# Optimization experiments

Measured on AMD Instinct MI355X. Metric: run time of the kernel, lower is better.

The kernel has to match this reference:

```python
import jax, jax.numpy as jnp
import numpy as np

N = 100000        # nodes
E_RAND = 1600000  # random edges (self loops appended -> E = E_RAND + N)
H = 64            # agg_hidden
IN = 7            # in_channels
L = 3             # n_layer
FC = 128          # fc_hidden
C = 2             # num_classes
G = 256           # graphs in the batch
SLOPE = 0.2       # GATv2 LeakyReLU negative slope


def _gatv2(x, src, dst, Wl, bl, Wr, br, att, bias):
    # GATv2Conv, heads=1, concat=True, no edge_attr
    xl = x @ Wl.T + bl                                      # [N,H] source transform
    xr = x @ Wr.T + br                                      # [N,H] target transform
    e = jax.nn.leaky_relu(xl[src] + xr[dst], SLOPE) @ att   # [E] per-edge score
    m = jax.ops.segment_max(e, dst, num_segments=N)         # segment softmax over in-edges
    w = jnp.exp(e - m[dst])
    denom = jax.ops.segment_sum(w, dst, num_segments=N)
    alpha = w / denom[dst]                                  # self loops guarantee denom > 0
    out = jax.ops.segment_sum(alpha[:, None] * xl[src], dst, num_segments=N)
    return out + bias


def _forward(x, eps, m0, v0, mrest, vrest, fc1_W, fc1_b, fc2_W, fc2_b, edge_index, batch):
    src, dst = edge_index[0], edge_index[1]
    mean = jax.nn.elu(_gatv2(x, src, dst, *m0))
    log_var = jax.nn.elu(_gatv2(x, src, dst, *v0))
    for i in range(L - 1):  # dropout is a no-op in eval mode
        mean = jax.nn.elu(_gatv2(mean, src, dst, *[p[i] for p in mrest]))
        log_var = jax.nn.elu(_gatv2(log_var, src, dst, *[p[i] for p in vrest]))
    z = mean + eps * jnp.exp(0.5 * log_var)                 # reparameterize
    counts = jax.ops.segment_sum(jnp.ones((N,), z.dtype), batch, num_segments=G)
    zg = jax.ops.segment_sum(z, batch, num_segments=G) / counts[:, None]  # global_mean_pool
    h = jax.nn.relu(zg @ fc1_W.T + fc1_b)
    logits = h @ fc2_W.T + fc2_b
    return jax.nn.log_softmax(logits, axis=1), mean, log_var


def setup_inputs() -> dict:
    key = jax.random.key(0)
    ks = iter(jax.random.split(key, 48))

    def nrm(shape, s=0.1):
        return s * jax.random.normal(next(ks), shape, jnp.float32)

    x = jax.random.normal(next(ks), (N, IN), jnp.float32)
    src = jax.random.randint(next(ks), (E_RAND,), 0, N)
    dst = jax.random.randint(next(ks), (E_RAND,), 0, N)
    loops = jnp.arange(N)
    edge_index = jnp.stack([jnp.concatenate([src, loops]),
                            jnp.concatenate([dst, loops])])  # add_self_loops=True
    batch = jnp.sort(jax.random.randint(next(ks), (N,), 0, G))
    eps = jax.random.normal(next(ks), (N, H), jnp.float32)

    d = dict(x=x, eps=eps, edge_index=edge_index, batch=batch)
    for pre, din in (("m0", IN), ("v0", IN)):
        d[pre + "_Wl"] = nrm((H, din)); d[pre + "_bl"] = nrm((H,))
        d[pre + "_Wr"] = nrm((H, din)); d[pre + "_br"] = nrm((H,))
        d[pre + "_att"] = nrm((H,));    d[pre + "_bias"] = nrm((H,))
    for pre in ("m", "v"):  # stacked hidden layers [L-1, ...]
        d[pre + "_Wl"] = nrm((L - 1, H, H)); d[pre + "_bl"] = nrm((L - 1, H))
        d[pre + "_Wr"] = nrm((L - 1, H, H)); d[pre + "_br"] = nrm((L - 1, H))
        d[pre + "_att"] = nrm((L - 1, H));   d[pre + "_bias"] = nrm((L - 1, H))
    d["fc1_W"] = nrm((FC, H)); d["fc1_b"] = nrm((FC,))
    d["fc2_W"] = nrm((C, FC)); d["fc2_b"] = nrm((C,))
    return d


def reference(x, eps, edge_index, batch,
              m0_Wl, m0_bl, m0_Wr, m0_br, m0_att, m0_bias,
              v0_Wl, v0_bl, v0_Wr, v0_br, v0_att, v0_bias,
              m_Wl, m_bl, m_Wr, m_br, m_att, m_bias,
              v_Wl, v_bl, v_Wr, v_br, v_att, v_bias,
              fc1_W, fc1_b, fc2_W, fc2_b):
    m0 = (m0_Wl, m0_bl, m0_Wr, m0_br, m0_att, m0_bias)
    v0 = (v0_Wl, v0_bl, v0_Wr, v0_br, v0_att, v0_bias)
    mrest = (m_Wl, m_bl, m_Wr, m_br, m_att, m_bias)
    vrest = (v_Wl, v_bl, v_Wr, v_br, v_att, v_bias)
    return _forward(x, eps, m0, v0, mrest, vrest, fc1_W, fc1_b, fc2_W, fc2_b, edge_index, batch)
```

## Files before the change

### kernel.cpp

```cpp
#include <hip/hip_runtime.h>
#include <hip/hip_fp16.h>
#include <math.h>


#define BSH 7
#define BMSK ((1 << BSH) - 1)
#define CHUNK 4096
#define SNB 4096

typedef _Float16 h2 __attribute__((ext_vector_type(2)));
typedef _Float16 h8 __attribute__((ext_vector_type(8)));
typedef float f4 __attribute__((ext_vector_type(4)));

__device__ __forceinline__ float elu1(float v) {
    return v > 0.f ? v : (__expf(v) - 1.f);
}

__device__ __forceinline__ float exp2fast(float x) {
#if defined(__has_builtin)
#if __has_builtin(__builtin_amdgcn_exp2f)
    return __builtin_amdgcn_exp2f(x);
#else
    return exp2f(x);
#endif
#else
    return exp2f(x);
#endif
}

__device__ __forceinline__ float dot2f(h2 a, h2 b, float c) {
#if defined(__has_builtin)
#if __has_builtin(__builtin_amdgcn_fdot2)
    return __builtin_amdgcn_fdot2(a, b, c, false);
#else
    return fmaf((float)a.x, (float)b.x, fmaf((float)a.y, (float)b.y, c));
#endif
#else
    return fmaf((float)a.x, (float)b.x, fmaf((float)a.y, (float)b.y, c));
#endif
}

template <int CTRL>
__device__ __forceinline__ float dppf(float v) {
    int r = __builtin_amdgcn_update_dpp(0, __builtin_bit_cast(int, v), CTRL, 0xF, 0xF, true);
    return __builtin_bit_cast(float, r);
}


__global__ void k_hist_bucket(const int* __restrict__ dst, int E,
                              int* __restrict__ bcnt, int nbk) {
    __shared__ int h[1024];
    for (int i = threadIdx.x; i < 1024; i += blockDim.x) h[i] = 0;
    __syncthreads();
    int stride = gridDim.x * blockDim.x;
    for (int e = blockIdx.x * blockDim.x + threadIdx.x; e < E; e += stride)
        atomicAdd(&h[dst[e] >> BSH], 1);
    __syncthreads();
    for (int i = threadIdx.x; i < nbk; i += blockDim.x)
        if (h[i]) atomicAdd(&bcnt[i], h[i]);
}

__global__ void k_scan_buckets(const int* __restrict__ bcnt, int nbk, int* __restrict__ boff,
                               int* __restrict__ bfill, int* __restrict__ bin_cnt) {
    __shared__ int sh[1024];
    int t = threadIdx.x;
    if (t < nbk) bfill[t] = 0;
    if (t < 256) bin_cnt[t] = 0;
    int v = (t < nbk) ? bcnt[t] : 0;
    sh[t] = v;
    __syncthreads();
    for (int o = 1; o < 1024; o <<= 1) {
        int u = (t >= o) ? sh[t - o] : 0;
        __syncthreads();
        sh[t] += u;
        __syncthreads();
    }
    if (t < nbk) boff[t] = sh[t] - v;
    if (t == nbk - 1) boff[nbk] = sh[t];
}

__global__ __launch_bounds__(256) void k_binfill(
    const int* __restrict__ src, const int* __restrict__ dst, int E,
    const int* __restrict__ boff, int* __restrict__ bfill, int* __restrict__ pairs) {
    __shared__ int h[1024];
    __shared__ int sbase[1024];
    int c0 = blockIdx.x * CHUNK;
    int c1 = min(c0 + CHUNK, E);
    for (int i = threadIdx.x; i < 1024; i += 256) h[i] = 0;
    __syncthreads();
    for (int e = c0 + threadIdx.x; e < c1; e += 256)
        atomicAdd(&h[dst[e] >> BSH], 1);
    __syncthreads();
    for (int i = threadIdx.x; i < 1024; i += 256) {
        int c = h[i];
        sbase[i] = c ? (boff[i] + atomicAdd(&bfill[i], c)) : 0;
        h[i] = 0;
    }
    __syncthreads();
    for (int e = c0 + threadIdx.x; e < c1; e += 256) {
        int d = dst[e];
        int b = d >> BSH;
        int off = atomicAdd(&h[b], 1);
        pairs[sbase[b] + off] = (src[e] << BSH) | (d & BMSK);
    }
}

__global__ __launch_bounds__(256) void k_bucket_csr(
    const int* __restrict__ pairs, const int* __restrict__ boff,
    int* __restrict__ rowptr, int* __restrict__ col, int N, int E) {
    __shared__ int deg[128], fill[128], scan[128], base[128];
    int b = blockIdx.x;
    int e0 = boff[b], e1 = boff[b + 1];
    int t = threadIdx.x;
    if (t < 128) { deg[t] = 0; fill[t] = 0; }
    __syncthreads();
    for (int i = e0 + t; i < e1; i += 256)
        atomicAdd(&deg[pairs[i] & BMSK], 1);
    __syncthreads();
    if (t < 128) scan[t] = deg[t];
    __syncthreads();
    for (int o = 1; o < 128; o <<= 1) {
        int u = (t >= o && t < 128) ? scan[t - o] : 0;
        __syncthreads();
        if (t < 128) scan[t] += u;
        __syncthreads();
    }
    if (t < 128) {
        int excl = e0 + scan[t] - deg[t];
        int node = (b << BSH) + t;
        if (node < N) rowptr[node] = excl;
        if (node == N - 1) rowptr[N] = E;
        base[t] = excl;
    }
    __syncthreads();
    for (int i = e0 + t; i < e1; i += 256) {
        int pk = pairs[i];
        int d = pk & BMSK;
        int pos = base[d] + atomicAdd(&fill[d], 1);
        col[pos] = ((unsigned)pk) >> BSH;
    }
}


__global__ __launch_bounds__(256) void k_deg_hist(const int* __restrict__ rowptr, int n,
                                                  int* __restrict__ bin_cnt,
                                                  int* __restrict__ blk_base) {
    __shared__ int h[256];
    h[threadIdx.x] = 0;
    __syncthreads();
    int b0 = blockIdx.x * SNB;
    int b1 = min(b0 + SNB, n);
    for (int i = b0 + threadIdx.x; i < b1; i += 256) {
        int d = 255 - min(rowptr[i + 1] - rowptr[i], 255);
        atomicAdd(&h[d], 1);
    }
    __syncthreads();
    int c = h[threadIdx.x];
    blk_base[blockIdx.x * 256 + threadIdx.x] = c ? atomicAdd(&bin_cnt[threadIdx.x], c) : 0;
}

__global__ void k_scan256(const int* __restrict__ bin_cnt, int* __restrict__ bin_off,
                          float* __restrict__ zsum, int G) {
    __shared__ int sh[256];
    int t = threadIdx.x;
    for (int i = t; i < G * 64; i += 256) zsum[i] = 0.f;
    int v = bin_cnt[t];
    sh[t] = v;
    __syncthreads();
    for (int o = 1; o < 256; o <<= 1) {
        int u = (t >= o) ? sh[t - o] : 0;
        __syncthreads();
        sh[t] += u;
        __syncthreads();
    }
    bin_off[t] = sh[t] - v;
}

__global__ __launch_bounds__(256) void k_deg_scatter(const int* __restrict__ rowptr, int n,
                                                     const int* __restrict__ bin_off,
                                                     const int* __restrict__ blk_base,
                                                     int* __restrict__ nodeof) {
    __shared__ int h[256];
    h[threadIdx.x] = 0;
    __syncthreads();
    int b0 = blockIdx.x * SNB;
    int b1 = min(b0 + SNB, n);
    for (int i = b0 + threadIdx.x; i < b1; i += 256) {
        int d = 255 - min(rowptr[i + 1] - rowptr[i], 255);
        int my = atomicAdd(&h[d], 1);
        nodeof[bin_off[d] + blk_base[blockIdx.x * 256 + d] + my] = i;
    }
}


__global__ void k_transform7(const float* __restrict__ X,
                             const float* __restrict__ mWl, const float* __restrict__ mbl,
                             const float* __restrict__ mWr, const float* __restrict__ mbr,
                             const float* __restrict__ vWl, const float* __restrict__ vbl,
                             const float* __restrict__ vWr, const float* __restrict__ vbr,
                             __half* __restrict__ xlb, __half* __restrict__ xrb, int n) {
    int t = blockIdx.x * blockDim.x + threadIdx.x;
    int node = t >> 6;
    if (node >= n) return;
    int h = t & 63;
    float aml = mbl[h], amr = mbr[h], avl = vbl[h], avr = vbr[h];
#pragma unroll
    for (int k = 0; k < 7; ++k) {
        float xv = X[node * 7 + k];
        aml = fmaf(xv, mWl[h * 7 + k], aml);
        amr = fmaf(xv, mWr[h * 7 + k], amr);
        avl = fmaf(xv, vWl[h * 7 + k], avl);
        avr = fmaf(xv, vWr[h * 7 + k], avr);
    }
    size_t o = (size_t)node * 128;
    xlb[o + h] = __float2half(aml);
    xlb[o + 64 + h] = __float2half(avl);
    xrb[o + h] = __float2half(amr);
    xrb[o + 64 + h] = __float2half(avr);
}

template <bool HIN>
__global__ __launch_bounds__(256) void k_transform_mfma2(
    const void* __restrict__ Xm, const void* __restrict__ Xv,
    const float* __restrict__ mWl, const float* __restrict__ mbl,
    const float* __restrict__ mWr, const float* __restrict__ mbr,
    const float* __restrict__ vWl, const float* __restrict__ vbl,
    const float* __restrict__ vWr, const float* __restrict__ vbr,
    __half* __restrict__ xlb, __half* __restrict__ xrb, int n) {
    int brn = blockIdx.y;
    const void* X   = brn ? Xv : Xm;
    const float* Wl = brn ? vWl : mWl;
    const float* bl = brn ? vbl : mbl;
    const float* Wr = brn ? vWr : mWr;
    const float* br = brn ? vbr : mbr;
    int base = brn * 64;

    __shared__ float biasLds[128];
    {
        int t = threadIdx.x;
        if (t < 64) biasLds[t] = bl[t];
        else if (t < 128) biasLds[t] = br[t - 64];
    }
    __syncthreads();
    int lane = threadIdx.x & 63;
    int l16 = lane & 15, lhi = lane >> 4;

    h8 aW[2][8];
    const float* Wp0 = Wl + (size_t)l16 * 64 + lhi * 8;
    const float* Wp1 = Wr + (size_t)l16 * 64 + lhi * 8;
#pragma unroll
    for (int tl = 0; tl < 4; ++tl) {
#pragma unroll
        for (int c = 0; c < 2; ++c) {
            const float* p0 = Wp0 + (size_t)tl * 16 * 64 + c * 32;
            const float* p1 = Wp1 + (size_t)tl * 16 * 64 + c * 32;
            float4 u0 = *(const float4*)p0, u1 = *(const float4*)(p0 + 4);
            float4 v0 = *(const float4*)p1, v1 = *(const float4*)(p1 + 4);
            h8 a0 = {(_Float16)u0.x, (_Float16)u0.y, (_Float16)u0.z, (_Float16)u0.w,
                     (_Float16)u1.x, (_Float16)u1.y, (_Float16)u1.z, (_Float16)u1.w};
            h8 a1 = {(_Float16)v0.x, (_Float16)v0.y, (_Float16)v0.z, (_Float16)v0.w,
                     (_Float16)v1.x, (_Float16)v1.y, (_Float16)v1.z, (_Float16)v1.w};
            aW[0][tl * 2 + c] = a0;
            aW[1][tl * 2 + c] = a1;
        }
    }

    int ntiles = (n + 15) >> 4;
    int wtile = blockIdx.x * 4 + (threadIdx.x >> 6);
    int wstride = gridDim.x * 4;
    for (int tile = wtile; tile < ntiles; tile += wstride) {
        int nb = tile * 16;
        int node = nb + l16;
        int nload = min(node, n - 1);
        h8 Bf[2];
#pragma unroll
        for (int c = 0; c < 2; ++c) {
            if (HIN) {
                const __half* p = (const __half*)X + (size_t)nload * 64 + c * 32 + lhi * 8;
                Bf[c] = *(const h8*)p;
            } else {
                const float* p = (const float*)X + (size_t)nload * 64 + c * 32 + lhi * 8;
                float4 u0 = *(const float4*)p, u1 = *(const float4*)(p + 4);
                h8 b = {(_Float16)u0.x, (_Float16)u0.y, (_Float16)u0.z, (_Float16)u0.w,
                        (_Float16)u1.x, (_Float16)u1.y, (_Float16)u1.z, (_Float16)u1.w};
                Bf[c] = b;
            }
        }
        f4 acc[2][4];
#pragma unroll
        for (int m = 0; m < 2; ++m)
#pragma unroll
            for (int tl = 0; tl < 4; ++tl) {
                f4 a = {0.f, 0.f, 0.f, 0.f};
                a = __builtin_amdgcn_mfma_f32_16x16x32_f16(aW[m][tl * 2 + 0], Bf[0], a, 0, 0, 0);
                a = __builtin_amdgcn_mfma_f32_16x16x32_f16(aW[m][tl * 2 + 1], Bf[1], a, 0, 0, 0);
                acc[m][tl] = a;
            }
        if (node < n) {
#pragma unroll
            for (int m = 0; m < 2; ++m) {
                __half* op = (m ? xrb : xlb) + (size_t)node * 128 + base;
#pragma unroll
                for (int tl = 0; tl < 4; ++tl) {
                    float4 bb = *(const float4*)&biasLds[m * 64 + tl * 16 + 4 * lhi];
                    h2 lo = {(_Float16)(acc[m][tl][0] + bb.x), (_Float16)(acc[m][tl][1] + bb.y)};
                    h2 hi = {(_Float16)(acc[m][tl][2] + bb.z), (_Float16)(acc[m][tl][3] + bb.w)};
                    uint2 pk = {*(unsigned*)&lo, *(unsigned*)&hi};
                    *(uint2*)(op + tl * 16 + 4 * lhi) = pk;
                }
            }
        }
    }
}


template <bool HOUT>
__global__ __launch_bounds__(256) void k_aggregate2(
    const __half* __restrict__ xlb, const __half* __restrict__ xrb,
    const float* __restrict__ attm, const float* __restrict__ attv,
    const float* __restrict__ biasm, const float* __restrict__ biasv,
    const int* __restrict__ rowptr, const int* __restrict__ col,
    const int* __restrict__ nodeof,
    void* __restrict__ outm, void* __restrict__ outv, int n) {
    int t = blockIdx.x * blockDim.x + threadIdx.x;
    int gid = t >> 4;
    if (gid >= n) return;
    int node = nodeof[gid];
    int l = t & 15;
    int s = l & 7;
    bool isv = l >= 8;

    int4 xri = ((const int4*)(xrb + (size_t)node * 128))[l];
    h2 xr0 = *(h2*)&xri.x, xr1 = *(h2*)&xri.y, xr2 = *(h2*)&xri.z, xr3 = *(h2*)&xri.w;
    const float* ap = (isv ? attv : attm) + s * 8;
    float4 af0 = *(const float4*)ap, af1 = *(const float4*)(ap + 4);
    const float C6 = 0.6f * 1.44269504f;
    const float C4 = 0.4f * 1.44269504f;
    h2 a6_0 = {(_Float16)(af0.x * C6), (_Float16)(af0.y * C6)};
    h2 a6_1 = {(_Float16)(af0.z * C6), (_Float16)(af0.w * C6)};
    h2 a6_2 = {(_Float16)(af1.x * C6), (_Float16)(af1.y * C6)};
    h2 a6_3 = {(_Float16)(af1.z * C6), (_Float16)(af1.w * C6)};
    h2 a4_0 = {(_Float16)(af0.x * C4), (_Float16)(af0.y * C4)};
    h2 a4_1 = {(_Float16)(af0.z * C4), (_Float16)(af0.w * C4)};
    h2 a4_2 = {(_Float16)(af1.x * C4), (_Float16)(af1.y * C4)};
    h2 a4_3 = {(_Float16)(af1.z * C4), (_Float16)(af1.w * C4)};

    float ac0 = 0.f, ac1 = 0.f, ac2 = 0.f, ac3 = 0.f;
    float ac4 = 0.f, ac5 = 0.f, ac6 = 0.f, ac7 = 0.f;
    float ssum = 0.f;

    auto proc = [&](int4 qi) {
        h2 x0 = *(h2*)&qi.x, x1 = *(h2*)&qi.y, x2 = *(h2*)&qi.z, x3 = *(h2*)&qi.w;
        h2 y0 = x0 + xr0, y1 = x1 + xr1, y2 = x2 + xr2, y3 = x3 + xr3;
        int z0i = (*(int*)&y0) & 0x7FFF7FFF;
        int z1i = (*(int*)&y1) & 0x7FFF7FFF;
        int z2i = (*(int*)&y2) & 0x7FFF7FFF;
        int z3i = (*(int*)&y3) & 0x7FFF7FFF;
        h2 z0 = *(h2*)&z0i, z1 = *(h2*)&z1i, z2 = *(h2*)&z2i, z3 = *(h2*)&z3i;
        float sc = dot2f(y0, a6_0, 0.f);
        float sa = dot2f(z0, a4_0, 0.f);
        sc = dot2f(y1, a6_1, sc);
        sa = dot2f(z1, a4_1, sa);
        sc = dot2f(y2, a6_2, sc);
        sa = dot2f(z2, a4_2, sa);
        sc = dot2f(y3, a6_3, sc);
        sa = dot2f(z3, a4_3, sa);
        sc += sa;
        sc += dppf<0xB1>(sc);
        sc += dppf<0x4E>(sc);
        sc += dppf<0x141>(sc);
        float w = exp2fast(sc);
        ssum += w;
        ac0 = fmaf(w, (float)x0.x, ac0);
        ac1 = fmaf(w, (float)x0.y, ac1);
        ac2 = fmaf(w, (float)x1.x, ac2);
        ac3 = fmaf(w, (float)x1.y, ac3);
        ac4 = fmaf(w, (float)x2.x, ac4);
        ac5 = fmaf(w, (float)x2.y, ac5);
        ac6 = fmaf(w, (float)x3.x, ac6);
        ac7 = fmaf(w, (float)x3.y, ac7);
    };

    int r0 = rowptr[node], r1 = rowptr[node + 1];
    const int4* xp = (const int4*)xlb + l;
    int last = r1 - 1;
    int nb = (r1 - r0) >> 2;
    int e = r0;
    int t0 = 0, t1 = 0, t2 = 0, t3 = 0;
    int4 qA0, qA1, qA2, qA3;
    if (nb) {
        int s0 = col[e], s1 = col[e + 1], s2 = col[e + 2], s3 = col[e + 3];
        qA0 = xp[(size_t)s0 * 16]; qA1 = xp[(size_t)s1 * 16];
        qA2 = xp[(size_t)s2 * 16]; qA3 = xp[(size_t)s3 * 16];
        int p = e + 4;
        t0 = col[min(p, last)];     t1 = col[min(p + 1, last)];
        t2 = col[min(p + 2, last)]; t3 = col[min(p + 3, last)];
    }
    for (int b = 0; b < nb; ++b) {
        int4 qB0, qB1, qB2, qB3;
        bool more = (b + 1 < nb);
        if (more) {
            qB0 = xp[(size_t)t0 * 16]; qB1 = xp[(size_t)t1 * 16];
            qB2 = xp[(size_t)t2 * 16]; qB3 = xp[(size_t)t3 * 16];
            int p = e + 8;
            t0 = col[min(p, last)];     t1 = col[min(p + 1, last)];
            t2 = col[min(p + 2, last)]; t3 = col[min(p + 3, last)];
        }
        proc(qA0); proc(qA1); proc(qA2); proc(qA3);
        if (more) { qA0 = qB0; qA1 = qB1; qA2 = qB2; qA3 = qB3; }
        e += 4;
    }
    for (e = r0 + nb * 4; e < r1; ++e)
        proc(xp[(size_t)col[e] * 16]);

    float inv = 1.f / ssum;
    const float* bp = (isv ? biasv : biasm) + s * 8;
    float4 b0 = *(const float4*)bp, b1 = *(const float4*)(bp + 4);
    float r00 = elu1(fmaf(ac0, inv, b0.x));
    float r01 = elu1(fmaf(ac1, inv, b0.y));
    float r02 = elu1(fmaf(ac2, inv, b0.z));
    float r03 = elu1(fmaf(ac3, inv, b0.w));
    float r04 = elu1(fmaf(ac4, inv, b1.x));
    float r05 = elu1(fmaf(ac5, inv, b1.y));
    float r06 = elu1(fmaf(ac6, inv, b1.z));
    float r07 = elu1(fmaf(ac7, inv, b1.w));
    if (HOUT) {
        __half* op = (__half*)(isv ? outv : outm) + (size_t)node * 64 + s * 8;
        h2 p0 = {(_Float16)r00, (_Float16)r01}, p1 = {(_Float16)r02, (_Float16)r03};
        h2 p2 = {(_Float16)r04, (_Float16)r05}, p3 = {(_Float16)r06, (_Float16)r07};
        uint4 pk = {*(unsigned*)&p0, *(unsigned*)&p1, *(unsigned*)&p2, *(unsigned*)&p3};
        *(uint4*)op = pk;
    } else {
        float* op = (float*)(isv ? outv : outm) + (size_t)node * 64 + s * 8;
        float4 r0v = {r00, r01, r02, r03};
        float4 r1v = {r04, r05, r06, r07};
        *(float4*)op = r0v;
        *(float4*)(op + 4) = r1v;
    }
}


__global__ void k_zpool(const float* __restrict__ mean, const float* __restrict__ logvar,
                        const float* __restrict__ eps, const int* __restrict__ batch,
                        float* __restrict__ zsum, int n) {
    int wave = blockIdx.x * 4 + (threadIdx.x >> 6);
    int lane = threadIdx.x & 63;
    int n0 = wave * 16;
    if (n0 >= n) return;
    int n1 = min(n0 + 16, n);
    float acc = 0.f;
    int gcur = -1;
    for (int nd = n0; nd < n1; ++nd) {
        int g = batch[nd];
        if (g != gcur) {
            if (gcur >= 0) atomicAdd(&zsum[gcur * 64 + lane], acc);
            gcur = g; acc = 0.f;
        }
        size_t o = (size_t)nd * 64 + lane;
        acc += fmaf(eps[o], __expf(0.5f * logvar[o]), mean[o]);
    }
    if (gcur >= 0) atomicAdd(&zsum[gcur * 64 + lane], acc);
}


__global__ void k_fchead(const float* __restrict__ zsum, const int* __restrict__ batch,
                         int N,
                         const float* __restrict__ fc1W, const float* __restrict__ fc1b,
                         const float* __restrict__ fc2W, const float* __restrict__ fc2b,
                         float* __restrict__ out) {
    __shared__ float zg[64];
    __shared__ float h1[128];
    __shared__ float lg[2];
    __shared__ int bnd[2];
    int g = blockIdx.x;
    int t = threadIdx.x;
    if (t < 2) {
        int tgt = g + t, lo = 0, hi = N;
        while (lo < hi) {
            int m = (lo + hi) >> 1;
            if (batch[m] < tgt) lo = m + 1; else hi = m;
        }
        bnd[t] = lo;
    }
    __syncthreads();
    float cntg = (float)(bnd[1] - bnd[0]);
    if (t < 64) zg[t] = zsum[g * 64 + t] / cntg;
    __syncthreads();
    float h = fc1b[t];
#pragma unroll
    for (int k = 0; k < 64; ++k) h = fmaf(zg[k], fc1W[t * 64 + k], h);
    h1[t] = fmaxf(h, 0.f);
    __syncthreads();
    if (t < 2) {
        float l = fc2b[t];
        for (int k = 0; k < 128; ++k) l = fmaf(h1[k], fc2W[t * 128 + k], l);
        lg[t] = l;
    }
    __syncthreads();
    if (t == 0) {
        float mx = fmaxf(lg[0], lg[1]);
        float lse = mx + logf(expf(lg[0] - mx) + expf(lg[1] - mx));
        out[g * 2 + 0] = lg[0] - lse;
        out[g * 2 + 1] = lg[1] - lse;
    }
}


extern "C" void kernel_launch(void* const* d_in, const int* in_sizes, int n_in,
                              void* d_out, int out_size, void* d_ws, size_t ws_size,
                              hipStream_t stream) {
    const float* x     = (const float*)d_in[0];
    const float* eps   = (const float*)d_in[1];
    const int*   eidx  = (const int*)d_in[2];
    const int*   batch = (const int*)d_in[3];
    const float* m0_Wl = (const float*)d_in[4];
    const float* m0_bl = (const float*)d_in[5];
    const float* m0_Wr = (const float*)d_in[6];
    const float* m0_br = (const float*)d_in[7];
    const float* m0_att = (const float*)d_in[8];
    const float* m0_bias = (const float*)d_in[9];
    const float* v0_Wl = (const float*)d_in[10];
    const float* v0_bl = (const float*)d_in[11];
    const float* v0_Wr = (const float*)d_in[12];
    const float* v0_br = (const float*)d_in[13];
    const float* v0_att = (const float*)d_in[14];
    const float* v0_bias = (const float*)d_in[15];
    const float* m_Wl = (const float*)d_in[16];
    const float* m_bl = (const float*)d_in[17];
    const float* m_Wr = (const float*)d_in[18];
    const float* m_br = (const float*)d_in[19];
    const float* m_att = (const float*)d_in[20];
    const float* m_bias = (const float*)d_in[21];
    const float* v_Wl = (const float*)d_in[22];
    const float* v_bl = (const float*)d_in[23];
    const float* v_Wr = (const float*)d_in[24];
    const float* v_br = (const float*)d_in[25];
    const float* v_att = (const float*)d_in[26];
    const float* v_bias = (const float*)d_in[27];
    const float* fc1W = (const float*)d_in[28];
    const float* fc1b = (const float*)d_in[29];
    const float* fc2W = (const float*)d_in[30];
    const float* fc2b = (const float*)d_in[31];

    const int N = in_sizes[1] / 64;
    const int E = in_sizes[2] / 2;
    const int G = (out_size - N * 128) / 2;
    const int nbk = (N + (1 << BSH) - 1) >> BSH;
    const int nsb = (N + SNB - 1) / SNB;
    const int* srcp = eidx;
    const int* dstp = eidx + E;

    char* wsb = (char*)d_ws;
    size_t off = 0;
    auto carve = [&](size_t bytes) -> void* {
        void* p = wsb + off;
        off += (bytes + 255) & ~(size_t)255;
        return p;
    };
    int*    rowptr   = (int*)carve((size_t)(N + 1) * sizeof(int));
    int*    col      = (int*)carve((size_t)E * sizeof(int));
    int*    pairs    = (int*)carve((size_t)E * sizeof(int));
    int*    bcnt     = (int*)carve((size_t)(nbk + 1) * sizeof(int));
    int*    boff     = (int*)carve((size_t)(nbk + 1) * sizeof(int));
    int*    bfill    = (int*)carve((size_t)nbk * sizeof(int));
    int*    nodeof   = (int*)carve((size_t)N * sizeof(int));
    int*    bin_cnt  = (int*)carve(256 * sizeof(int));
    int*    bin_off  = (int*)carve(256 * sizeof(int));
    int*    blk_base = (int*)carve((size_t)nsb * 256 * sizeof(int));
    __half* xlb      = (__half*)carve((size_t)N * 128 * sizeof(__half));
    __half* xrb      = (__half*)carve((size_t)N * 128 * sizeof(__half));
    __half* meanh    = (__half*)carve((size_t)N * 64 * sizeof(__half));
    __half* logvarh  = (__half*)carve((size_t)N * 64 * sizeof(__half));
    float*  zsum     = (float*)carve((size_t)G * 64 * sizeof(float));
    (void)ws_size;

    float* out_logits = (float*)d_out;
    float* mean_buf   = out_logits + (size_t)G * 2;
    float* logvar_buf = mean_buf + (size_t)N * 64;

    const int agrid = (N * 16 + 255) / 256;
    const int tgrid7 = (N * 64 + 255) / 256;
    const int mgrid = ((N + 15) / 16 + 3) / 4;
    const int zgrid = ((N + 15) / 16 + 3) / 4;

    (void)hipMemsetAsync(bcnt, 0, (size_t)nbk * sizeof(int), stream);
    k_hist_bucket<<<256, 256, 0, stream>>>(dstp, E, bcnt, nbk);
    k_scan_buckets<<<1, 1024, 0, stream>>>(bcnt, nbk, boff, bfill, bin_cnt);
    k_binfill<<<(E + CHUNK - 1) / CHUNK, 256, 0, stream>>>(srcp, dstp, E, boff, bfill, pairs);
    k_bucket_csr<<<nbk, 256, 0, stream>>>(pairs, boff, rowptr, col, N, E);

    k_deg_hist<<<nsb, 256, 0, stream>>>(rowptr, N, bin_cnt, blk_base);
    k_scan256<<<1, 256, 0, stream>>>(bin_cnt, bin_off, zsum, G);
    k_deg_scatter<<<nsb, 256, 0, stream>>>(rowptr, N, bin_off, blk_base, nodeof);

    k_transform7<<<tgrid7, 256, 0, stream>>>(x, m0_Wl, m0_bl, m0_Wr, m0_br,
                                             v0_Wl, v0_bl, v0_Wr, v0_br, xlb, xrb, N);
    k_aggregate2<true><<<agrid, 256, 0, stream>>>(xlb, xrb, m0_att, v0_att, m0_bias, v0_bias,
                                                  rowptr, col, nodeof, meanh, logvarh, N);

    for (int l = 0; l < 2; ++l) {
        k_transform_mfma2<true><<<dim3(mgrid, 2), 256, 0, stream>>>(
            meanh, logvarh,
            m_Wl + (size_t)l * 4096, m_bl + l * 64, m_Wr + (size_t)l * 4096, m_br + l * 64,
            v_Wl + (size_t)l * 4096, v_bl + l * 64, v_Wr + (size_t)l * 4096, v_br + l * 64,
            xlb, xrb, N);
        if (l == 0)
            k_aggregate2<true><<<agrid, 256, 0, stream>>>(
                xlb, xrb, m_att + l * 64, v_att + l * 64, m_bias + l * 64, v_bias + l * 64,
                rowptr, col, nodeof, meanh, logvarh, N);
        else
            k_aggregate2<false><<<agrid, 256, 0, stream>>>(
                xlb, xrb, m_att + l * 64, v_att + l * 64, m_bias + l * 64, v_bias + l * 64,
                rowptr, col, nodeof, mean_buf, logvar_buf, N);
    }

    k_zpool<<<zgrid, 256, 0, stream>>>(mean_buf, logvar_buf, eps, batch, zsum, N);
    k_fchead<<<G, 128, 0, stream>>>(zsum, batch, N, fc1W, fc1b, fc2W, fc2b, out_logits);
}
```

Measured before the change: 462.2 us.

## Fuse reparameterize and mean-pool into final aggregate kernel via per-node atomics

```diff
diff --git a/kernel.cpp b/kernel.cpp
--- a/kernel.cpp
+++ b/kernel.cpp
@@ -219,16 +219,15 @@
     xrb[o + 64 + h] = __float2half(avr);
 }
 
-template <bool HIN>
 __global__ __launch_bounds__(256) void k_transform_mfma2(
-    const void* __restrict__ Xm, const void* __restrict__ Xv,
+    const __half* __restrict__ Xm, const __half* __restrict__ Xv,
     const float* __restrict__ mWl, const float* __restrict__ mbl,
     const float* __restrict__ mWr, const float* __restrict__ mbr,
     const float* __restrict__ vWl, const float* __restrict__ vbl,
     const float* __restrict__ vWr, const float* __restrict__ vbr,
     __half* __restrict__ xlb, __half* __restrict__ xrb, int n) {
     int brn = blockIdx.y;
-    const void* X   = brn ? Xv : Xm;
+    const __half* X = brn ? Xv : Xm;
     const float* Wl = brn ? vWl : mWl;
     const float* bl = brn ? vbl : mbl;
     const float* Wr = brn ? vWr : mWr;
@@ -275,16 +274,8 @@
         h8 Bf[2];
 #pragma unroll
         for (int c = 0; c < 2; ++c) {
-            if (HIN) {
-                const __half* p = (const __half*)X + (size_t)nload * 64 + c * 32 + lhi * 8;
-                Bf[c] = *(const h8*)p;
-            } else {
-                const float* p = (const float*)X + (size_t)nload * 64 + c * 32 + lhi * 8;
-                float4 u0 = *(const float4*)p, u1 = *(const float4*)(p + 4);
-                h8 b = {(_Float16)u0.x, (_Float16)u0.y, (_Float16)u0.z, (_Float16)u0.w,
-                        (_Float16)u1.x, (_Float16)u1.y, (_Float16)u1.z, (_Float16)u1.w};
-                Bf[c] = b;
-            }
+            const __half* p = X + (size_t)nload * 64 + c * 32 + lhi * 8;
+            Bf[c] = *(const h8*)p;
         }
         f4 acc[2][4];
 #pragma unroll
@@ -314,14 +305,16 @@
 }
 
 
-template <bool HOUT>
+template <bool HOUT, bool FUSE>
 __global__ __launch_bounds__(256) void k_aggregate2(
     const __half* __restrict__ xlb, const __half* __restrict__ xrb,
     const float* __restrict__ attm, const float* __restrict__ attv,
     const float* __restrict__ biasm, const float* __restrict__ biasv,
     const int* __restrict__ rowptr, const int* __restrict__ col,
     const int* __restrict__ nodeof,
-    void* __restrict__ outm, void* __restrict__ outv, int n) {
+    void* __restrict__ outm, void* __restrict__ outv, int n,
+    const float* __restrict__ eps, const int* __restrict__ batch,
+    float* __restrict__ zsum) {
     int t = blockIdx.x * blockDim.x + threadIdx.x;
     int gid = t >> 4;
     if (gid >= n) return;
@@ -437,29 +430,27 @@
         *(float4*)op = r0v;
         *(float4*)(op + 4) = r1v;
     }
-}
-
-
-__global__ void k_zpool(const float* __restrict__ mean, const float* __restrict__ logvar,
-                        const float* __restrict__ eps, const int* __restrict__ batch,
-                        float* __restrict__ zsum, int n) {
-    int wave = blockIdx.x * 4 + (threadIdx.x >> 6);
-    int lane = threadIdx.x & 63;
-    int n0 = wave * 16;
-    if (n0 >= n) return;
-    int n1 = min(n0 + 16, n);
-    float acc = 0.f;
-    int gcur = -1;
-    for (int nd = n0; nd < n1; ++nd) {
-        int g = batch[nd];
-        if (g != gcur) {
-            if (gcur >= 0) atomicAdd(&zsum[gcur * 64 + lane], acc);
-            gcur = g; acc = 0.f;
+
+    if (FUSE) {
+        float lv0 = __shfl_xor(r00, 8), lv1 = __shfl_xor(r01, 8);
+        float lv2 = __shfl_xor(r02, 8), lv3 = __shfl_xor(r03, 8);
+        float lv4 = __shfl_xor(r04, 8), lv5 = __shfl_xor(r05, 8);
+        float lv6 = __shfl_xor(r06, 8), lv7 = __shfl_xor(r07, 8);
+        if (!isv) {
+            int g = batch[node];
+            const float* ep = eps + (size_t)node * 64 + s * 8;
+            float4 e0 = *(const float4*)ep, e1 = *(const float4*)(ep + 4);
+            float* zp = zsum + (size_t)g * 64 + s * 8;
+            atomicAdd(zp + 0, fmaf(e0.x, __expf(0.5f * lv0), r00));
+            atomicAdd(zp + 1, fmaf(e0.y, __expf(0.5f * lv1), r01));
+            atomicAdd(zp + 2, fmaf(e0.z, __expf(0.5f * lv2), r02));
+            atomicAdd(zp + 3, fmaf(e0.w, __expf(0.5f * lv3), r03));
+            atomicAdd(zp + 4, fmaf(e1.x, __expf(0.5f * lv4), r04));
+            atomicAdd(zp + 5, fmaf(e1.y, __expf(0.5f * lv5), r05));
+            atomicAdd(zp + 6, fmaf(e1.z, __expf(0.5f * lv6), r06));
+            atomicAdd(zp + 7, fmaf(e1.w, __expf(0.5f * lv7), r07));
         }
-        size_t o = (size_t)nd * 64 + lane;
-        acc += fmaf(eps[o], __expf(0.5f * logvar[o]), mean[o]);
-    }
-    if (gcur >= 0) atomicAdd(&zsum[gcur * 64 + lane], acc);
+    }
 }
 
 
@@ -580,8 +571,8 @@
 
     const int agrid = (N * 16 + 255) / 256;
     const int tgrid7 = (N * 64 + 255) / 256;
-    const int mgrid = ((N + 15) / 16 + 3) / 4;
-    const int zgrid = ((N + 15) / 16 + 3) / 4;
+    const int ntiles = (N + 15) / 16;
+    const int mgrid = (ntiles + 15) / 16;
 
     (void)hipMemsetAsync(bcnt, 0, (size_t)nbk * sizeof(int), stream);
     k_hist_bucket<<<256, 256, 0, stream>>>(dstp, E, bcnt, nbk);
@@ -595,25 +586,25 @@
 
     k_transform7<<<tgrid7, 256, 0, stream>>>(x, m0_Wl, m0_bl, m0_Wr, m0_br,
                                              v0_Wl, v0_bl, v0_Wr, v0_br, xlb, xrb, N);
-    k_aggregate2<true><<<agrid, 256, 0, stream>>>(xlb, xrb, m0_att, v0_att, m0_bias, v0_bias,
-                                                  rowptr, col, nodeof, meanh, logvarh, N);
+    k_aggregate2<true, false><<<agrid, 256, 0, stream>>>(
+        xlb, xrb, m0_att, v0_att, m0_bias, v0_bias,
+        rowptr, col, nodeof, meanh, logvarh, N, nullptr, nullptr, nullptr);
 
     for (int l = 0; l < 2; ++l) {
-        k_transform_mfma2<true><<<dim3(mgrid, 2), 256, 0, stream>>>(
+        k_transform_mfma2<<<dim3(mgrid, 2), 256, 0, stream>>>(
             meanh, logvarh,
             m_Wl + (size_t)l * 4096, m_bl + l * 64, m_Wr + (size_t)l * 4096, m_br + l * 64,
             v_Wl + (size_t)l * 4096, v_bl + l * 64, v_Wr + (size_t)l * 4096, v_br + l * 64,
             xlb, xrb, N);
         if (l == 0)
-            k_aggregate2<true><<<agrid, 256, 0, stream>>>(
+            k_aggregate2<true, false><<<agrid, 256, 0, stream>>>(
                 xlb, xrb, m_att + l * 64, v_att + l * 64, m_bias + l * 64, v_bias + l * 64,
-                rowptr, col, nodeof, meanh, logvarh, N);
+                rowptr, col, nodeof, meanh, logvarh, N, nullptr, nullptr, nullptr);
         else
-            k_aggregate2<false><<<agrid, 256, 0, stream>>>(
+            k_aggregate2<false, true><<<agrid, 256, 0, stream>>>(
                 xlb, xrb, m_att + l * 64, v_att + l * 64, m_bias + l * 64, v_bias + l * 64,
-                rowptr, col, nodeof, mean_buf, logvar_buf, N);
-    }
-
-    k_zpool<<<zgrid, 256, 0, stream>>>(mean_buf, logvar_buf, eps, batch, zsum, N);
+                rowptr, col, nodeof, mean_buf, logvar_buf, N, eps, batch, zsum);
+    }
+
     k_fchead<<<G, 128, 0, stream>>>(zsum, batch, N, fc1W, fc1b, fc2W, fc2b, out_logits);
 }
```

Result: slower. 658.2 us (+42.4%).
